# Optimization experiments

Hardware: AMD Instinct MI355X
Metric: run time of the kernel (lower is better)

## Reference

```python
import jax, jax.numpy as jnp
import numpy as np

B, F, E = 2048, 24, 128
P = F * (F - 1) // 2  # 276 upper-triangular field pairs


def setup_inputs() -> dict:
    key = jax.random.key(0)
    k1, k2 = jax.random.split(key)
    x = jax.random.normal(k1, (B, F, E), dtype=jnp.float32)
    # keras random_normal initializer uses small stddev; 0.05 mirrors that
    kernel = jax.random.normal(k2, (E, P, E), dtype=jnp.float32) * 0.05
    return {"x": x, "kernel": kernel}


def reference(x, kernel):
    F_ = x.shape[1]
    p_idx, q_idx = np.triu_indices(F_, k=1)  # static pair index lists (i < j)
    Xp = x[:, p_idx, :]  # [B, P, E]
    Xq = x[:, q_idx, :]  # [B, P, E]
    # result[b,p] = sum_{d,e} Xp[b,p,e] * kernel[d,p,e] * Xq[b,p,d]
    # fused einsum avoids the [B, E, P, E] intermediate the TF code materializes
    result = jnp.einsum("bpe,dpe,bpd->bp", Xp, kernel, Xq)
    return result
```

## Files before the change

### kernel.cpp

```cpp
#include <hip/hip_runtime.h>
#include <stdint.h>

#define B_SZ 2048
#define F_SZ 24
#define E_SZ 128
#define P_SZ 276
#define BT   256
#define NWG  (P_SZ * 8)

#define XT_ELEMS (B_SZ * F_SZ * E_SZ)
#define KB_ELEMS (P_SZ * E_SZ * E_SZ)
#define WS_NEED  ((size_t)(2 * XT_ELEMS + KB_ELEMS) * 2)

#define XPREP_BLKS (F_SZ * 64)
#define KPREP_BLKS (KB_ELEMS / 2048)

typedef __bf16 bf16x8 __attribute__((ext_vector_type(8)));
typedef __bf16 bf16x4 __attribute__((ext_vector_type(4)));
typedef float  f32x16 __attribute__((ext_vector_type(16)));

__global__ __launch_bounds__(256) void prepack_all(
    const float* __restrict__ x, const float* __restrict__ kern,
    __bf16* __restrict__ xft, __bf16* __restrict__ xqt, __bf16* __restrict__ kb)
{
    const int bid = blockIdx.x;
    const int tid = threadIdx.x;
    if (bid < XPREP_BLKS) {
        const int f = bid >> 6, grp = bid & 63;
        __shared__ float sT[32][129];
        {
            const int row = tid >> 3, c0 = (tid & 7) * 16;
            const float* src = x + ((size_t)(grp * 32 + row) * F_SZ + f) * E_SZ + c0;
            float4 v0 = ((const float4*)src)[0];
            float4 v1 = ((const float4*)src)[1];
            float4 v2 = ((const float4*)src)[2];
            float4 v3 = ((const float4*)src)[3];
            *(float4*)&sT[row][c0]      = v0;
            *(float4*)&sT[row][c0 + 4]  = v1;
            *(float4*)&sT[row][c0 + 8]  = v2;
            *(float4*)&sT[row][c0 + 12] = v3;
        }
        __syncthreads();
        {
            __bf16* dst = xft + ((size_t)(f * 64 + grp) * 8) * 512;
#pragma unroll
            for (int u = 0; u < 2; ++u) {
                const int slot = tid * 2 + u;
                const int kk = slot >> 6, lane = slot & 63;
                const int l31 = lane & 31, hi = lane >> 5;
                bf16x8 h;
#pragma unroll
                for (int i = 0; i < 8; ++i)
                    h[i] = (__bf16)sT[l31][kk * 16 + hi * 8 + i];
                *(bf16x8*)(dst + slot * 8) = h;
            }
        }
        {
            __bf16* dst = xqt + ((size_t)(f * 64 + grp) * 32) * 128;
#pragma unroll
            for (int u = 0; u < 4; ++u) {
                const int slot = tid * 4 + u;
                const int dq = slot >> 5, bl = slot & 31;
                bf16x4 h;
#pragma unroll
                for (int i = 0; i < 4; ++i)
                    h[i] = (__bf16)sT[bl][dq * 4 + i];
                *(bf16x4*)(dst + slot * 4) = h;
            }
        }
    } else {
        int g = (bid - XPREP_BLKS) * 256 + tid;
        int p = g >> 11, r = g & 2047;
        int d = r >> 4, s = r & 15;
        const float* src = kern + ((size_t)d * P_SZ + p) * E_SZ + ((s ^ (d & 15)) << 3);
        float4 v0 = *(const float4*)src;
        float4 v1 = *(const float4*)(src + 4);
        bf16x8 h;
        h[0] = (__bf16)v0.x; h[1] = (__bf16)v0.y; h[2] = (__bf16)v0.z; h[3] = (__bf16)v0.w;
        h[4] = (__bf16)v1.x; h[5] = (__bf16)v1.y; h[6] = (__bf16)v1.z; h[7] = (__bf16)v1.w;
        *(bf16x8*)(kb + (size_t)g * 8) = h;
    }
}

__global__ __launch_bounds__(512, 4) void opn_main(
    const __bf16* __restrict__ xft, const __bf16* __restrict__ xqt,
    const __bf16* __restrict__ kb,  float* __restrict__ out)
{
    __shared__ short sK[E_SZ * E_SZ];

    const int tid = threadIdx.x, w = tid >> 6, lane = tid & 63;
    const int l31 = lane & 31, hi = lane >> 5;
    const int orig = blockIdx.x;
    const int bb = orig & 7;
    const int p  = orig >> 3;

    int fp = 0, rem = p;
    while (rem >= F_SZ - 1 - fp) { rem -= F_SZ - 1 - fp; ++fp; }
    const int fq = fp + 1 + rem;

    const __bf16* kp = kb + (size_t)p * (E_SZ * E_SZ);
#pragma unroll
    for (int t = 0; t < 4; ++t) {
        const int base = (w * 4 + t) * 64;
        __builtin_amdgcn_global_load_lds(
            (const __attribute__((address_space(1))) void*)(kp + (size_t)(base + lane) * 8),
            (__attribute__((address_space(3))) void*)(&sK[base * 8]),
            16, 0, 0);
    }

    const int grp = bb * 8 + w;
    bf16x8 xpf[8];
    const __bf16* xpb = xft + ((size_t)(fp * 64 + grp) * 8) * 512 + lane * 8;
#pragma unroll
    for (int kk = 0; kk < 8; ++kk)
        xpf[kk] = *(const bf16x8*)(xpb + kk * 512);

    __syncthreads();

    f32x16 acc[4];
#pragma unroll
    for (int mt = 0; mt < 4; ++mt)
#pragma unroll
        for (int q = 0; q < 16; ++q) acc[mt][q] = 0.f;

#pragma unroll
    for (int kk = 0; kk < 8; ++kk) {
        const int e8 = kk * 2 + hi;
#pragma unroll
        for (int mt = 0; mt < 4; ++mt) {
            const int arow = mt * 32 + l31;
            bf16x8 afr = *(const bf16x8*)&sK[arow * E_SZ + ((e8 ^ (arow & 15)) << 3)];
            acc[mt] = __builtin_amdgcn_mfma_f32_32x32x16_bf16(afr, xpf[kk], acc[mt], 0, 0, 0);
        }
    }

    const __bf16* xqb = xqt + ((size_t)(fq * 64 + grp) * 32) * 128 + hi * 128 + l31 * 4;
    float s0 = 0.f, s1 = 0.f;
#pragma unroll
    for (int mt = 0; mt < 4; ++mt) {
        bf16x4 xq0 = *(const bf16x4*)(xqb + (size_t)(mt * 8 + 0) * 128);
        bf16x4 xq1 = *(const bf16x4*)(xqb + (size_t)(mt * 8 + 2) * 128);
        bf16x4 xq2 = *(const bf16x4*)(xqb + (size_t)(mt * 8 + 4) * 128);
        bf16x4 xq3 = *(const bf16x4*)(xqb + (size_t)(mt * 8 + 6) * 128);
        s0 += acc[mt][ 0] * (float)xq0[0] + acc[mt][ 1] * (float)xq0[1]
            + acc[mt][ 2] * (float)xq0[2] + acc[mt][ 3] * (float)xq0[3];
        s1 += acc[mt][ 4] * (float)xq1[0] + acc[mt][ 5] * (float)xq1[1]
            + acc[mt][ 6] * (float)xq1[2] + acc[mt][ 7] * (float)xq1[3];
        s0 += acc[mt][ 8] * (float)xq2[0] + acc[mt][ 9] * (float)xq2[1]
            + acc[mt][10] * (float)xq2[2] + acc[mt][11] * (float)xq2[3];
        s1 += acc[mt][12] * (float)xq3[0] + acc[mt][13] * (float)xq3[1]
            + acc[mt][14] * (float)xq3[2] + acc[mt][15] * (float)xq3[3];
    }
    float s = s0 + s1;
    s += __shfl_xor(s, 32);
    if (hi == 0)
        out[(size_t)(grp * 32 + l31) * P_SZ + p] = s;
}

__global__ __launch_bounds__(512, 4) void opn_fallback(
    const float* __restrict__ x, const float* __restrict__ kern,
    float* __restrict__ out)
{
    __shared__ short sA[128 * E_SZ];
    __shared__ short sB[E_SZ * E_SZ];
    __shared__ float red[2][128];

    const int tid = threadIdx.x;
    const int orig = blockIdx.x;
    const int nwg2 = P_SZ * 16;
    const int wgid = (orig & 7) * (nwg2 / 8) + (orig >> 3);
    const int p  = wgid >> 4;
    const int bb = wgid & 15;
    const int b0 = bb * 128;

    int fp = 0, rem = p;
    while (rem >= F_SZ - 1 - fp) { rem -= F_SZ - 1 - fp; ++fp; }
    const int fq = fp + 1 + rem;

#pragma unroll
    for (int k = 0; k < 4; ++k) {
        int i = tid + k * 512;
        int r = i >> 4, s8 = i & 15;
        const float* src = x + ((size_t)(b0 + r) * F_SZ + fp) * E_SZ + s8 * 8;
        float4 v0 = *(const float4*)src;
        float4 v1 = *(const float4*)(src + 4);
        bf16x8 h;
        h[0] = (__bf16)v0.x; h[1] = (__bf16)v0.y; h[2] = (__bf16)v0.z; h[3] = (__bf16)v0.w;
        h[4] = (__bf16)v1.x; h[5] = (__bf16)v1.y; h[6] = (__bf16)v1.z; h[7] = (__bf16)v1.w;
        *(bf16x8*)&sA[r * E_SZ + ((s8 ^ (r & 15)) << 3)] = h;
    }
#pragma unroll
    for (int k = 0; k < 4; ++k) {
        int i = tid + k * 512;
        int r = i >> 4, s8 = i & 15;
        const float* src = kern + ((size_t)r * P_SZ + p) * E_SZ + s8 * 8;
        float4 v0 = *(const float4*)src;
        float4 v1 = *(const float4*)(src + 4);
        bf16x8 h;
        h[0] = (__bf16)v0.x; h[1] = (__bf16)v0.y; h[2] = (__bf16)v0.z; h[3] = (__bf16)v0.w;
        h[4] = (__bf16)v1.x; h[5] = (__bf16)v1.y; h[6] = (__bf16)v1.z; h[7] = (__bf16)v1.w;
        *(bf16x8*)&sB[r * E_SZ + ((s8 ^ (r & 15)) << 3)] = h;
    }
    __syncthreads();

    const int w = tid >> 6, lane = tid & 63;
    const int l31 = lane & 31, hi = lane >> 5;
    const int mh = w >> 2, ng = w & 3;

    f32x16 acc[2];
#pragma unroll
    for (int mt = 0; mt < 2; ++mt)
#pragma unroll
        for (int j = 0; j < 16; ++j) acc[mt][j] = 0.f;

    const int brow = ng * 32 + l31;
#pragma unroll
    for (int kk = 0; kk < 8; ++kk) {
        const int e8 = kk * 2 + hi;
        bf16x8 bfr = *(const bf16x8*)&sA[brow * E_SZ + ((e8 ^ (brow & 15)) << 3)];
#pragma unroll
        for (int mt = 0; mt < 2; ++mt) {
            int arow = (mh * 2 + mt) * 32 + l31;
            bf16x8 afr = *(const bf16x8*)&sB[arow * E_SZ + ((e8 ^ (arow & 15)) << 3)];
            acc[mt] = __builtin_amdgcn_mfma_f32_32x32x16_bf16(afr, bfr, acc[mt], 0, 0, 0);
        }
    }

    const float* xqp = x + ((size_t)(b0 + brow) * F_SZ + fq) * E_SZ;
    float sv = 0.f;
#pragma unroll
    for (int mt = 0; mt < 2; ++mt) {
        const int dbase = (mh * 2 + mt) * 32 + hi * 4;
#pragma unroll
        for (int q = 0; q < 4; ++q) {
            float4 xq = *(const float4*)(xqp + dbase + q * 8);
            sv += acc[mt][q * 4 + 0] * xq.x + acc[mt][q * 4 + 1] * xq.y
                + acc[mt][q * 4 + 2] * xq.z + acc[mt][q * 4 + 3] * xq.w;
        }
    }
    sv += __shfl_xor(sv, 32);
    if (hi == 0) red[mh][brow] = sv;
    __syncthreads();

    if (tid < 128)
        out[(size_t)(b0 + tid) * P_SZ + p] = red[0][tid] + red[1][tid];
}

extern "C" void kernel_launch(void* const* d_in, const int* in_sizes, int n_in,
                              void* d_out, int out_size, void* d_ws, size_t ws_size,
                              hipStream_t stream) {
    const float* x    = (const float*)d_in[0];
    const float* kern = (const float*)d_in[1];
    float* out = (float*)d_out;

    if (ws_size >= WS_NEED) {
        __bf16* xft = (__bf16*)d_ws;
        __bf16* xqt = xft + XT_ELEMS;
        __bf16* kb  = xqt + XT_ELEMS;
        prepack_all<<<dim3(XPREP_BLKS + KPREP_BLKS), 256, 0, stream>>>(x, kern, xft, xqt, kb);
        opn_main<<<dim3(NWG), 512, 0, stream>>>(xft, xqt, kb, out);
    } else {
        opn_fallback<<<dim3(P_SZ * 16), 512, 0, stream>>>(x, kern, out);
    }
}
```

Before: 45.85 us.

## Drop separate Xq transposed buffer and reuse Xp layout for both operands

The prepack kernel no longer builds a second transposed bf16 copy of x or stages through shared memory. It converts x directly into the MFMA B-fragment layout, and the main kernel reads its Xq values out of that same buffer with a remapped index. The main kernel also prefetches all Xq values into registers before the barrier, accumulates one 32-row M tile at a time so fewer accumulator registers are live, and sets a cache-policy bit on the LDS-direct kernel loads. This cuts prepack writes and workspace traffic, at the cost of less coalesced direct global reads of x in the prepack.

```diff
diff --git a/kernel.cpp b/kernel.cpp
--- a/kernel.cpp
+++ b/kernel.cpp
@@ -10,7 +10,7 @@
 
 #define XT_ELEMS (B_SZ * F_SZ * E_SZ)
 #define KB_ELEMS (P_SZ * E_SZ * E_SZ)
-#define WS_NEED  ((size_t)(2 * XT_ELEMS + KB_ELEMS) * 2)
+#define WS_NEED  ((size_t)(XT_ELEMS + KB_ELEMS) * 2)
 
 #define XPREP_BLKS (F_SZ * 64)
 #define KPREP_BLKS (KB_ELEMS / 2048)
@@ -21,52 +21,26 @@
 
 __global__ __launch_bounds__(256) void prepack_all(
     const float* __restrict__ x, const float* __restrict__ kern,
-    __bf16* __restrict__ xft, __bf16* __restrict__ xqt, __bf16* __restrict__ kb)
+    __bf16* __restrict__ xft, __bf16* __restrict__ kb)
 {
     const int bid = blockIdx.x;
     const int tid = threadIdx.x;
     if (bid < XPREP_BLKS) {
         const int f = bid >> 6, grp = bid & 63;
-        __shared__ float sT[32][129];
-        {
-            const int row = tid >> 3, c0 = (tid & 7) * 16;
-            const float* src = x + ((size_t)(grp * 32 + row) * F_SZ + f) * E_SZ + c0;
-            float4 v0 = ((const float4*)src)[0];
-            float4 v1 = ((const float4*)src)[1];
-            float4 v2 = ((const float4*)src)[2];
-            float4 v3 = ((const float4*)src)[3];
-            *(float4*)&sT[row][c0]      = v0;
-            *(float4*)&sT[row][c0 + 4]  = v1;
-            *(float4*)&sT[row][c0 + 8]  = v2;
-            *(float4*)&sT[row][c0 + 12] = v3;
-        }
-        __syncthreads();
-        {
-            __bf16* dst = xft + ((size_t)(f * 64 + grp) * 8) * 512;
-#pragma unroll
-            for (int u = 0; u < 2; ++u) {
-                const int slot = tid * 2 + u;
-                const int kk = slot >> 6, lane = slot & 63;
-                const int l31 = lane & 31, hi = lane >> 5;
-                bf16x8 h;
-#pragma unroll
-                for (int i = 0; i < 8; ++i)
-                    h[i] = (__bf16)sT[l31][kk * 16 + hi * 8 + i];
-                *(bf16x8*)(dst + slot * 8) = h;
-            }
-        }
-        {
-            __bf16* dst = xqt + ((size_t)(f * 64 + grp) * 32) * 128;
-#pragma unroll
-            for (int u = 0; u < 4; ++u) {
-                const int slot = tid * 4 + u;
-                const int dq = slot >> 5, bl = slot & 31;
-                bf16x4 h;
-#pragma unroll
-                for (int i = 0; i < 4; ++i)
-                    h[i] = (__bf16)sT[bl][dq * 4 + i];
-                *(bf16x4*)(dst + slot * 4) = h;
-            }
+        const float* srcb = x + ((size_t)grp * 32 * F_SZ + f) * E_SZ;
+        __bf16* dst = xft + (size_t)(f * 64 + grp) * 4096;
+#pragma unroll
+        for (int u = 0; u < 2; ++u) {
+            const int s = tid * 2 + u;
+            const int row = s & 31;
+            const int e0  = (s >> 6) * 16 + ((s >> 5) & 1) * 8;
+            const float* src = srcb + (size_t)row * (F_SZ * E_SZ) + e0;
+            float4 v0 = *(const float4*)src;
+            float4 v1 = *(const float4*)(src + 4);
+            bf16x8 h;
+            h[0] = (__bf16)v0.x; h[1] = (__bf16)v0.y; h[2] = (__bf16)v0.z; h[3] = (__bf16)v0.w;
+            h[4] = (__bf16)v1.x; h[5] = (__bf16)v1.y; h[6] = (__bf16)v1.z; h[7] = (__bf16)v1.w;
+            *(bf16x8*)(dst + s * 8) = h;
         }
     } else {
         int g = (bid - XPREP_BLKS) * 256 + tid;
@@ -83,8 +57,8 @@
 }
 
 __global__ __launch_bounds__(512, 4) void opn_main(
-    const __bf16* __restrict__ xft, const __bf16* __restrict__ xqt,
-    const __bf16* __restrict__ kb,  float* __restrict__ out)
+    const __bf16* __restrict__ xft, const __bf16* __restrict__ kb,
+    float* __restrict__ out)
 {
     __shared__ short sK[E_SZ * E_SZ];
 
@@ -105,51 +79,45 @@
         __builtin_amdgcn_global_load_lds(
             (const __attribute__((address_space(1))) void*)(kp + (size_t)(base + lane) * 8),
             (__attribute__((address_space(3))) void*)(&sK[base * 8]),
-            16, 0, 0);
+            16, 0, 2 );
     }
 
     const int grp = bb * 8 + w;
     bf16x8 xpf[8];
-    const __bf16* xpb = xft + ((size_t)(fp * 64 + grp) * 8) * 512 + lane * 8;
+    const __bf16* xpb = xft + (size_t)(fp * 64 + grp) * 4096 + lane * 8;
 #pragma unroll
     for (int kk = 0; kk < 8; ++kk)
         xpf[kk] = *(const bf16x8*)(xpb + kk * 512);
+    bf16x4 xqr[4][4];
+    const __bf16* xqb = xft + (size_t)(fq * 64 + grp) * 4096 + l31 * 8 + hi * 4;
+#pragma unroll
+    for (int mt = 0; mt < 4; ++mt)
+#pragma unroll
+        for (int q = 0; q < 4; ++q)
+            xqr[mt][q] = *(const bf16x4*)(xqb + (mt * 2 + (q >> 1)) * 512 + (q & 1) * 256);
 
     __syncthreads();
 
-    f32x16 acc[4];
-#pragma unroll
-    for (int mt = 0; mt < 4; ++mt)
-#pragma unroll
-        for (int q = 0; q < 16; ++q) acc[mt][q] = 0.f;
-
-#pragma unroll
-    for (int kk = 0; kk < 8; ++kk) {
-        const int e8 = kk * 2 + hi;
-#pragma unroll
-        for (int mt = 0; mt < 4; ++mt) {
-            const int arow = mt * 32 + l31;
-            bf16x8 afr = *(const bf16x8*)&sK[arow * E_SZ + ((e8 ^ (arow & 15)) << 3)];
-            acc[mt] = __builtin_amdgcn_mfma_f32_32x32x16_bf16(afr, xpf[kk], acc[mt], 0, 0, 0);
-        }
-    }
-
-    const __bf16* xqb = xqt + ((size_t)(fq * 64 + grp) * 32) * 128 + hi * 128 + l31 * 4;
     float s0 = 0.f, s1 = 0.f;
 #pragma unroll
     for (int mt = 0; mt < 4; ++mt) {
-        bf16x4 xq0 = *(const bf16x4*)(xqb + (size_t)(mt * 8 + 0) * 128);
-        bf16x4 xq1 = *(const bf16x4*)(xqb + (size_t)(mt * 8 + 2) * 128);
-        bf16x4 xq2 = *(const bf16x4*)(xqb + (size_t)(mt * 8 + 4) * 128);
-        bf16x4 xq3 = *(const bf16x4*)(xqb + (size_t)(mt * 8 + 6) * 128);
-        s0 += acc[mt][ 0] * (float)xq0[0] + acc[mt][ 1] * (float)xq0[1]
-            + acc[mt][ 2] * (float)xq0[2] + acc[mt][ 3] * (float)xq0[3];
-        s1 += acc[mt][ 4] * (float)xq1[0] + acc[mt][ 5] * (float)xq1[1]
-            + acc[mt][ 6] * (float)xq1[2] + acc[mt][ 7] * (float)xq1[3];
-        s0 += acc[mt][ 8] * (float)xq2[0] + acc[mt][ 9] * (float)xq2[1]
-            + acc[mt][10] * (float)xq2[2] + acc[mt][11] * (float)xq2[3];
-        s1 += acc[mt][12] * (float)xq3[0] + acc[mt][13] * (float)xq3[1]
-            + acc[mt][14] * (float)xq3[2] + acc[mt][15] * (float)xq3[3];
+        f32x16 acc;
+#pragma unroll
+        for (int q = 0; q < 16; ++q) acc[q] = 0.f;
+        const int arow = mt * 32 + l31;
+        const short* kRow = &sK[arow * E_SZ];
+        const int asw = (arow & 15) << 3;
+#pragma unroll
+        for (int kk = 0; kk < 8; ++kk) {
+            bf16x8 afr = *(const bf16x8*)&kRow[((kk * 2 + hi) << 3) ^ asw];
+            acc = __builtin_amdgcn_mfma_f32_32x32x16_bf16(afr, xpf[kk], acc, 0, 0, 0);
+        }
+#pragma unroll
+        for (int q = 0; q < 4; ++q) {
+            const bf16x4 xq = xqr[mt][q];
+            s0 += acc[q * 4 + 0] * (float)xq[0] + acc[q * 4 + 1] * (float)xq[1];
+            s1 += acc[q * 4 + 2] * (float)xq[2] + acc[q * 4 + 3] * (float)xq[3];
+        }
     }
     float s = s0 + s1;
     s += __shfl_xor(s, 32);
@@ -255,10 +223,9 @@
 
     if (ws_size >= WS_NEED) {
         __bf16* xft = (__bf16*)d_ws;
-        __bf16* xqt = xft + XT_ELEMS;
-        __bf16* kb  = xqt + XT_ELEMS;
-        prepack_all<<<dim3(XPREP_BLKS + KPREP_BLKS), 256, 0, stream>>>(x, kern, xft, xqt, kb);
-        opn_main<<<dim3(NWG), 512, 0, stream>>>(xft, xqt, kb, out);
+        __bf16* kb  = xft + XT_ELEMS;
+        prepack_all<<<dim3(XPREP_BLKS + KPREP_BLKS), 256, 0, stream>>>(x, kern, xft, kb);
+        opn_main<<<dim3(NWG), 512, 0, stream>>>(xft, kb, out);
     } else {
         opn_fallback<<<dim3(P_SZ * 16), 512, 0, stream>>>(x, kern, out);
     }
```

Result: slower. 49.59 us (+8.2%).
